# Performance work log

Hardware: AMD Instinct MI355X
Metric: run time of the kernel (lower is better)

## Reference

```python
import jax, jax.numpy as jnp
import numpy as np

HIDDEN = 2048
N_HEADS = 32
N_KV = 4
HEAD_DIM = 128
EPS = 1e-6
THETA = 1e6
B, S = 2, 2048


def setup_inputs() -> dict:
    key = jax.random.key(0)
    k1, k2, k3 = jax.random.split(key, 3)
    hidden_states = jax.random.normal(k1, (B, S, HIDDEN), dtype=jnp.float32)
    positions = jnp.broadcast_to(jnp.arange(S, dtype=jnp.int32), (B, S))
    w_qkv = jax.random.normal(k2, ((N_HEADS + 2 * N_KV) * HEAD_DIM, HIDDEN), dtype=jnp.float32) * 0.02
    w_o = jax.random.normal(k3, (HIDDEN, N_HEADS * HEAD_DIM), dtype=jnp.float32) * 0.02
    q_norm_w = jnp.ones((HEAD_DIM,), dtype=jnp.float32)
    k_norm_w = jnp.ones((HEAD_DIM,), dtype=jnp.float32)
    return {"hidden_states": hidden_states, "positions": positions,
            "w_qkv": w_qkv, "w_o": w_o, "q_norm_w": q_norm_w, "k_norm_w": k_norm_w}


def _rms_norm(x, w):
    # x: [..., HEAD_DIM]
    var = jnp.mean(x * x, axis=-1, keepdims=True)
    return x * jax.lax.rsqrt(var + EPS) * w


def _rope(x, positions):
    # NEOX-style rotary. x: [B,S,H,D], positions: [B,S]
    half = HEAD_DIM // 2
    inv_freq = 1.0 / (THETA ** (jnp.arange(0, half, dtype=jnp.float32) / half))
    ang = positions.astype(jnp.float32)[..., None] * inv_freq  # [B,S,half]
    cos = jnp.cos(ang)[:, :, None, :]
    sin = jnp.sin(ang)[:, :, None, :]
    x1, x2 = x[..., :half], x[..., half:]
    return jnp.concatenate([x1 * cos - x2 * sin, x2 * cos + x1 * sin], axis=-1)


def reference(hidden_states, positions, w_qkv, w_o, q_norm_w, k_norm_w):
    q_size = N_HEADS * HEAD_DIM
    kv_size = N_KV * HEAD_DIM
    qkv = jnp.einsum('bsh,oh->bso', hidden_states, w_qkv)
    q = qkv[..., :q_size].reshape(B, S, N_HEADS, HEAD_DIM)
    k = qkv[..., q_size:q_size + kv_size].reshape(B, S, N_KV, HEAD_DIM)
    v = qkv[..., q_size + kv_size:].reshape(B, S, N_KV, HEAD_DIM)
    # per-head RMSNorm then RoPE
    q = _rope(_rms_norm(q, q_norm_w), positions)
    k = _rope(_rms_norm(k, k_norm_w), positions)
    rep = N_HEADS // N_KV
    k = jnp.repeat(k, rep, axis=2)
    v = jnp.repeat(v, rep, axis=2)
    scale = HEAD_DIM ** -0.5
    scores = jnp.einsum('bqhd,bkhd->bhqk', q, k) * scale
    causal = jnp.tril(jnp.ones((S, S), dtype=bool))
    scores = jnp.where(causal, scores, jnp.finfo(scores.dtype).min)
    probs = jax.nn.softmax(scores, axis=-1)
    attn = jnp.einsum('bhqk,bkhd->bqhd', probs, v).reshape(B, S, N_HEADS * HEAD_DIM)
    return jnp.einsum('bsa,ha->bsh', attn, w_o)
```

## Files before the change

kernel.cpp:

```cpp
#include <hip/hip_runtime.h>
#include <cstdint>

#define SEQ 2048
#define BATCH 2
#define NTOK 4096
#define HID 2048
#define NH 32
#define NKV 4
#define HD 128
#define QKV_O 5120

typedef __attribute__((ext_vector_type(8))) short short8;
typedef __attribute__((ext_vector_type(8))) unsigned short u16x8;
typedef __attribute__((ext_vector_type(4))) unsigned short u16x4;
typedef __attribute__((ext_vector_type(4))) float f32x4;

__device__ __forceinline__ float bf2f(unsigned short u) {
  union { unsigned int i; float f; } v; v.i = ((unsigned int)u) << 16; return v.f;
}
__device__ __forceinline__ unsigned short f2bf(float f) {
  union { float f; unsigned int i; } v; v.f = f;
  unsigned int r = v.i + 0x7FFFu + ((v.i >> 16) & 1u);
  return (unsigned short)(r >> 16);
}

__device__ __forceinline__ void load_lds16(const void* g, void* l) {
  __builtin_amdgcn_global_load_lds((const __attribute__((address_space(1))) unsigned int*)g,
                                   (__attribute__((address_space(3))) unsigned int*)l, 16, 0, 0);
}

__global__ __launch_bounds__(256) void convert_to_bf16(const float* __restrict__ src,
                                                       unsigned short* __restrict__ dst,
                                                       int n4) {
  int i = blockIdx.x * blockDim.x + threadIdx.x;
  int stride = gridDim.x * blockDim.x;
  for (; i < n4; i += stride) {
    f32x4 v = *(const f32x4*)(src + 4 * (size_t)i);
    u16x4 o;
    o.x = f2bf(v.x); o.y = f2bf(v.y); o.z = f2bf(v.z); o.w = f2bf(v.w);
    *(u16x4*)(dst + 4 * (size_t)i) = o;
  }
}

__global__ __launch_bounds__(256) void reduce_add(float* __restrict__ out,
                                                  const float* __restrict__ part, int n4) {
  int i = blockIdx.x * blockDim.x + threadIdx.x;
  int stride = gridDim.x * blockDim.x;
  for (; i < n4; i += stride) {
    f32x4 a = *(const f32x4*)(out + 4 * (size_t)i);
    f32x4 b = *(const f32x4*)(part + 4 * (size_t)i);
    a.x += b.x; a.y += b.y; a.z += b.z; a.w += b.w;
    *(f32x4*)(out + 4 * (size_t)i) = a;
  }
}

template <bool OUT_F32, bool SPLIT>
__global__ __launch_bounds__(512, 2) void gemm256(
    const unsigned short* __restrict__ A, const unsigned short* __restrict__ B,
    void* __restrict__ C0, void* __restrict__ C1,
    int lda, int ldb, int ldc, int Kloop) {
  __shared__ alignas(16) unsigned short As[2][256 * 64];
  __shared__ alignas(16) unsigned short Bs[2][256 * 64];

  const int t = threadIdx.x;
  const int lane = t & 63, w = t >> 6;
  const int fr = lane & 15, g = lane >> 4;
  const int wm = w >> 2, wn = w & 3;
  const size_t m0 = (size_t)blockIdx.y * 256;
  const size_t n0 = (size_t)blockIdx.x * 256;
  const int kbase = SPLIT ? (int)blockIdx.z * Kloop : 0;
  void* Cv = (SPLIT && blockIdx.z) ? C1 : C0;

  const int srow = w * 8 + (lane >> 3);
  const int sch = (lane & 7) ^ ((lane >> 3) & 7);
  const unsigned short* gA[4];
  const unsigned short* gB[4];
#pragma unroll
  for (int i = 0; i < 4; i++) {
    gA[i] = A + (m0 + i * 64 + srow) * (size_t)lda + kbase + sch * 8;
    gB[i] = B + (n0 + i * 64 + srow) * (size_t)ldb + kbase + sch * 8;
  }

  auto stage = [&](int k0, int bi) {
#pragma unroll
    for (int i = 0; i < 4; i++) {
      load_lds16(gA[i] + k0, &As[bi][(i * 512 + w * 64) * 8]);
      load_lds16(gB[i] + k0, &Bs[bi][(i * 512 + w * 64) * 8]);
    }
  };

  f32x4 acc[8][4] = {};
  stage(0, 0);

  const int nk = Kloop / 64;
  for (int kt = 0; kt < nk; kt++) {
    const int cur = kt & 1;
    asm volatile("s_waitcnt vmcnt(0)" ::: "memory");
    __builtin_amdgcn_s_barrier();
    __builtin_amdgcn_sched_barrier(0);
    if (kt + 1 < nk) stage((kt + 1) * 64, cur ^ 1);

    const unsigned short* Ac = As[cur];
    const unsigned short* Bc = Bs[cur];

    short8 bfr[4][2];
#pragma unroll
    for (int nf = 0; nf < 4; nf++) {
      const int row = wn * 64 + nf * 16 + fr;
#pragma unroll
      for (int s = 0; s < 2; s++)
        bfr[nf][s] = *(const short8*)&Bc[row * 64 + (((s * 4 + g) ^ (fr & 7)) * 8)];
    }
    __builtin_amdgcn_s_setprio(1);
#pragma unroll
    for (int mf = 0; mf < 8; mf++) {
      const int row = wm * 128 + mf * 16 + fr;
      short8 af0 = *(const short8*)&Ac[row * 64 + (((0 + g) ^ (fr & 7)) * 8)];
      short8 af1 = *(const short8*)&Ac[row * 64 + (((4 + g) ^ (fr & 7)) * 8)];
#pragma unroll
      for (int nf = 0; nf < 4; nf++) {
        acc[mf][nf] = __builtin_amdgcn_mfma_f32_16x16x32_bf16(af0, bfr[nf][0], acc[mf][nf], 0, 0, 0);
        acc[mf][nf] = __builtin_amdgcn_mfma_f32_16x16x32_bf16(af1, bfr[nf][1], acc[mf][nf], 0, 0, 0);
      }
    }
    __builtin_amdgcn_s_setprio(0);
  }

#pragma unroll
  for (int mf = 0; mf < 8; mf++)
#pragma unroll
    for (int nf = 0; nf < 4; nf++) {
      size_t row = m0 + wm * 128 + mf * 16 + g * 4;
      size_t col = n0 + wn * 64 + nf * 16 + fr;
#pragma unroll
      for (int r = 0; r < 4; r++) {
        if (OUT_F32) ((float*)Cv)[(row + r) * ldc + col] = acc[mf][nf][r];
        else ((unsigned short*)Cv)[(row + r) * ldc + col] = f2bf(acc[mf][nf][r]);
      }
    }
}

template <bool OUT_F32>
__global__ __launch_bounds__(256) void gemm_bt_bf16(
    const unsigned short* __restrict__ A, const unsigned short* __restrict__ B,
    void* __restrict__ Cv, int lda, int ldb, int ldc, int K) {
  __shared__ alignas(16) unsigned short As[128 * 32];
  __shared__ alignas(16) unsigned short Bs[128 * 32];

  const int t    = threadIdx.x;
  const int lane = t & 63;
  const int w    = t >> 6;
  const int wm   = (w >> 1) * 64;
  const int wn   = (w & 1) * 64;
  const size_t m0 = (size_t)blockIdx.y * 128;
  const size_t n0 = (size_t)blockIdx.x * 128;

  f32x4 acc[4][4] = {};

  const int srow = w * 32 + (lane >> 2);
  const int scol = (lane & 3) * 8;
  const unsigned short* gA0 = &A[(m0 + srow) * (size_t)lda + scol];
  const unsigned short* gA1 = gA0 + 16 * (size_t)lda;
  const unsigned short* gB0 = &B[(n0 + srow) * (size_t)ldb + scol];
  const unsigned short* gB1 = gB0 + 16 * (size_t)ldb;
  unsigned short* lA0 = &As[(w * 32) * 32];
  unsigned short* lA1 = &As[(w * 32 + 16) * 32];
  unsigned short* lB0 = &Bs[(w * 32) * 32];
  unsigned short* lB1 = &Bs[(w * 32 + 16) * 32];

  const int fr = lane & 15;
  const int kb = (lane >> 4) * 8;

  for (int k0 = 0; k0 < K; k0 += 32) {
    load_lds16(gA0 + k0, lA0);
    load_lds16(gA1 + k0, lA1);
    load_lds16(gB0 + k0, lB0);
    load_lds16(gB1 + k0, lB1);
    __syncthreads();
    short8 af[4], bf[4];
#pragma unroll
    for (int mt = 0; mt < 4; mt++) af[mt] = *(const short8*)&As[(wm + mt * 16 + fr) * 32 + kb];
#pragma unroll
    for (int nt = 0; nt < 4; nt++) bf[nt] = *(const short8*)&Bs[(wn + nt * 16 + fr) * 32 + kb];
#pragma unroll
    for (int mt = 0; mt < 4; mt++)
#pragma unroll
      for (int nt = 0; nt < 4; nt++)
        acc[mt][nt] = __builtin_amdgcn_mfma_f32_16x16x32_bf16(af[mt], bf[nt], acc[mt][nt], 0, 0, 0);
    __syncthreads();
  }

  const int r4 = (lane >> 4) * 4;
  const int cc = lane & 15;
#pragma unroll
  for (int mt = 0; mt < 4; mt++)
#pragma unroll
    for (int nt = 0; nt < 4; nt++) {
      size_t row = m0 + wm + mt * 16 + r4;
      size_t col = n0 + wn + nt * 16 + cc;
#pragma unroll
      for (int r = 0; r < 4; r++) {
        if (OUT_F32) ((float*)Cv)[(row + r) * ldc + col] = acc[mt][nt][r];
        else ((unsigned short*)Cv)[(row + r) * ldc + col] = f2bf(acc[mt][nt][r]);
      }
    }
}

__global__ __launch_bounds__(64) void rope_tab(const int* __restrict__ pos,
                                               float2* __restrict__ tab) {
  const int tok = blockIdx.x;
  const int j = threadIdx.x;
  float p = (float)pos[tok];
  float inv_freq = expf((float)j * (-13.815510557964274f / 64.0f));
  float ang = p * inv_freq;
  float2 cs; cs.x = cosf(ang); cs.y = sinf(ang);
  tab[tok * 64 + j] = cs;
}

__global__ __launch_bounds__(256) void normrope(
    unsigned short* __restrict__ qkv, const float2* __restrict__ tab,
    const unsigned short* __restrict__ qw, const unsigned short* __restrict__ kw) {
  const int wv   = threadIdx.x >> 6;
  const int lane = threadIdx.x & 63;
  const int h    = blockIdx.x * 4 + wv;
  const int tok  = blockIdx.z * SEQ + blockIdx.y;

  const unsigned short* w = (h < NH) ? qw : kw;
  const size_t src = (size_t)tok * QKV_O + (size_t)h * HD;

  float x1 = bf2f(qkv[src + lane]);
  float x2 = bf2f(qkv[src + lane + 64]);
  float ss = x1 * x1 + x2 * x2;
#pragma unroll
  for (int off = 32; off; off >>= 1) ss += __shfl_xor(ss, off);
  float r = rsqrtf(ss * (1.0f / 128.0f) + 1e-6f);
  float n1 = x1 * r * bf2f(w[lane]);
  float n2 = x2 * r * bf2f(w[lane + 64]);

  float2 cs = tab[tok * 64 + lane];
  qkv[src + lane]      = f2bf(n1 * cs.x - n2 * cs.y);
  qkv[src + lane + 64] = f2bf(n2 * cs.x + n1 * cs.y);
}

__global__ __launch_bounds__(256) void transpose_v(const unsigned short* __restrict__ qkv,
                                                   unsigned short* __restrict__ vt) {
  __shared__ alignas(16) unsigned short Vs[64][136];
  const int k0 = blockIdx.x * 64, kvh = blockIdx.y, b = blockIdx.z;
  const int t = threadIdx.x;
  const int voff = (NH + NKV) * HD + kvh * HD;
  {
    const int row = t >> 2, cb = (t & 3) * 8;
    const size_t gb = (size_t)(b * SEQ + k0 + row) * QKV_O + voff;
#pragma unroll
    for (int r = 0; r < 4; r++)
      *(uint4*)&Vs[row][cb + 32 * r] = *(const uint4*)&qkv[gb + cb + 32 * r];
  }
  __syncthreads();
  const int d = t >> 1, half = t & 1;
  const size_t ob = ((size_t)((b * NKV + kvh) * HD + d)) * SEQ + k0 + half * 32;
#pragma unroll
  for (int i = 0; i < 4; i++) {
    u16x8 vv;
#pragma unroll
    for (int j = 0; j < 8; j++) vv[j] = Vs[half * 32 + i * 8 + j][d];
    *(u16x8*)&vt[ob + i * 8] = vv;
  }
}

__global__ __launch_bounds__(512, 4) void flash_mfma(unsigned short* __restrict__ qkv,
                                                     const unsigned short* __restrict__ vt) {
  __shared__ alignas(16) unsigned short Kbuf[2][64 * 128];
  __shared__ alignas(16) unsigned short Vbuf[2][128 * 64];
  __shared__ alignas(16) unsigned short Ps[8][16 * 64];

  const int p = (int)blockIdx.x;
  const int h = blockIdx.y, b = blockIdx.z;
  const int t = threadIdx.x;
  const int lane = t & 63, w = t >> 6;
  const int c = lane & 15, g = lane >> 4;
  const int kvh = h >> 3;
  const int koff = NH * HD + kvh * HD;
  const float scale = 0.08838834764831845f;
  const int swz = c & 7;
  const int nqt = SEQ / 128;

  const int rK0 = t >> 4,         jK0 = (t & 15) ^ (rK0 & 15);
  const int rK1 = (t + 512) >> 4, jK1 = ((t + 512) & 15) ^ (rK1 & 15);
  const int dV0 = t >> 3,         jV0 = (t & 7) ^ (dV0 & 7);
  const int dV1 = (t + 512) >> 3, jV1 = ((t + 512) & 7) ^ (dV1 & 7);
  const unsigned short* gK0 = qkv + (size_t)(b * SEQ + rK0) * QKV_O + koff + jK0 * 8;
  const unsigned short* gK1 = qkv + (size_t)(b * SEQ + rK1) * QKV_O + koff + jK1 * 8;
  const unsigned short* gV0 = vt + ((size_t)(b * NKV + kvh) * HD + dV0) * SEQ + jV0 * 8;
  const unsigned short* gV1 = vt + ((size_t)(b * NKV + kvh) * HD + dV1) * SEQ + jV1 * 8;

  auto stage = [&](int k0s, int bi) {
    load_lds16(gK0 + (size_t)k0s * QKV_O, &Kbuf[bi][(w * 64) * 8]);
    load_lds16(gK1 + (size_t)k0s * QKV_O, &Kbuf[bi][(w * 64 + 512) * 8]);
    load_lds16(gV0 + k0s, &Vbuf[bi][(w * 64) * 8]);
    load_lds16(gV1 + k0s, &Vbuf[bi][(w * 64 + 512) * 8]);
  };

  for (int job = 0; job < 2; job++) {
    const int qt = job == 0 ? (nqt - 1 - p) : p;
    const int q0 = qt * 128;
    const int nkt = 2 * qt + 2;

    stage(0, 0);

    short8 qf[4];
    {
      const size_t qr = (size_t)(b * SEQ + q0 + w * 16 + c) * QKV_O + (size_t)h * HD;
#pragma unroll
      for (int ks = 0; ks < 4; ks++)
        qf[ks] = *(const short8*)&qkv[qr + ks * 32 + g * 8];
    }

    f32x4 O[8] = {};
    float m_i = -1e30f, l_i = 0.0f;

    for (int kt = 0; kt < nkt; kt++) {
      const int cur = kt & 1;
      asm volatile("s_waitcnt vmcnt(0)" ::: "memory");
      __builtin_amdgcn_s_barrier();
      __builtin_amdgcn_sched_barrier(0);
      if (kt + 1 < nkt) stage((kt + 1) * 64, cur ^ 1);

      const unsigned short* Kc = Kbuf[cur];
      const unsigned short* Vc = Vbuf[cur];

      f32x4 sc[4];
#pragma unroll
      for (int mt = 0; mt < 4; mt++) sc[mt] = (f32x4){0.f, 0.f, 0.f, 0.f};
      __builtin_amdgcn_s_setprio(1);
#pragma unroll
      for (int ks = 0; ks < 4; ks++) {
#pragma unroll
        for (int mt = 0; mt < 4; mt++) {
          short8 kf = *(const short8*)&Kc[(mt * 16 + c) * 128 + (((ks * 4 + g) ^ c) * 8)];
          sc[mt] = __builtin_amdgcn_mfma_f32_16x16x32_bf16(kf, qf[ks], sc[mt], 0, 0, 0);
        }
      }
      __builtin_amdgcn_s_setprio(0);

      const int k0 = kt * 64;
      const int qrow = q0 + w * 16 + c;
      const bool need_mask = (k0 + 63 > q0 + w * 16);
      float mx = -3.0e38f;
#pragma unroll
      for (int mt = 0; mt < 4; mt++)
#pragma unroll
        for (int r = 0; r < 4; r++) {
          float s = sc[mt][r];
          if (need_mask && (k0 + mt * 16 + g * 4 + r > qrow)) s = -3.0e38f;
          sc[mt][r] = s;
          mx = fmaxf(mx, s);
        }
      mx = fmaxf(mx, __shfl_xor(mx, 16));
      mx = fmaxf(mx, __shfl_xor(mx, 32));
      float mxs = mx * scale;

      if (!__all(mxs - m_i <= 8.0f)) {
        float m_new = fmaxf(m_i, mxs);
        float alpha = __expf(m_i - m_new);
        f32x4 a4;
#pragma unroll
        for (int r = 0; r < 4; r++) a4[r] = __shfl(alpha, g * 4 + r);
#pragma unroll
        for (int nt = 0; nt < 8; nt++)
#pragma unroll
          for (int r = 0; r < 4; r++) O[nt][r] *= a4[r];
        l_i *= alpha;
        m_i = m_new;
      }

      float psum = 0.0f;
#pragma unroll
      for (int mt = 0; mt < 4; mt++) {
        float pv[4];
#pragma unroll
        for (int r = 0; r < 4; r++) {
          pv[r] = __expf(__builtin_fmaf(sc[mt][r], scale, -m_i));
          psum += pv[r];
        }
        unsigned int pk0, pk1;
        asm("v_cvt_pk_bf16_f32 %0, %1, %2" : "=v"(pk0) : "v"(pv[0]), "v"(pv[1]));
        asm("v_cvt_pk_bf16_f32 %0, %1, %2" : "=v"(pk1) : "v"(pv[2]), "v"(pv[3]));
        uint2 pk; pk.x = pk0; pk.y = pk1;
        *(uint2*)&Ps[w][c * 64 + (((mt * 2 + (g >> 1)) ^ swz) * 8) + (g & 1) * 4] = pk;
      }
      psum += __shfl_xor(psum, 16);
      psum += __shfl_xor(psum, 32);
      l_i += psum;

      __builtin_amdgcn_s_setprio(1);
#pragma unroll
      for (int ks = 0; ks < 2; ks++) {
        short8 pf = *(const short8*)&Ps[w][c * 64 + (((ks * 4 + g) ^ swz) * 8)];
#pragma unroll
        for (int nt = 0; nt < 8; nt++) {
          short8 vf = *(const short8*)&Vc[(nt * 16 + c) * 64 + (((ks * 4 + g) ^ swz) * 8)];
          O[nt] = __builtin_amdgcn_mfma_f32_16x16x32_bf16(pf, vf, O[nt], 0, 0, 0);
        }
      }
      __builtin_amdgcn_s_setprio(0);
    }

    f32x4 l4;
#pragma unroll
    for (int r = 0; r < 4; r++) l4[r] = __shfl(l_i, g * 4 + r);
    f32x4 li;
#pragma unroll
    for (int r = 0; r < 4; r++) li[r] = 1.0f / l4[r];
#pragma unroll
    for (int nt = 0; nt < 8; nt++)
#pragma unroll
      for (int r = 0; r < 4; r++) {
        size_t addr = (size_t)(b * SEQ + q0 + w * 16 + g * 4 + r) * QKV_O + h * HD + nt * 16 + c;
        qkv[addr] = f2bf(O[nt][r] * li[r]);
      }
  }
}

extern "C" void kernel_launch(void* const* d_in, const int* in_sizes, int n_in,
                              void* d_out, int out_size, void* d_ws, size_t ws_size,
                              hipStream_t stream) {
  const float* hidden_f = (const float*)d_in[0];
  const int* positions  = (const int*)d_in[1];
  const float* wqkv_f   = (const float*)d_in[2];
  const float* wo_f     = (const float*)d_in[3];
  const float* qn_f     = (const float*)d_in[4];
  const float* kn_f     = (const float*)d_in[5];
  float* out            = (float*)d_out;

  char* ws = (char*)d_ws;
  unsigned short* hidden_c = (unsigned short*)ws;
  unsigned short* wqkv_c   = (unsigned short*)(ws + 16777216);
  unsigned short* wo_c     = (unsigned short*)(ws + 37748736);
  unsigned short* qn_c     = (unsigned short*)(ws + 54525952);
  unsigned short* kn_c     = (unsigned short*)(ws + 54526208);
  unsigned short* qkv      = (unsigned short*)(ws + 54526464);
  unsigned short* vt_g     = (unsigned short*)(ws + 96469504);
  float2* rtab             = (float2*)ws;
  float* p0                = (float*)ws;

  convert_to_bf16<<<1024, 256, 0, stream>>>(hidden_f, hidden_c, NTOK * HID / 4);
  convert_to_bf16<<<1024, 256, 0, stream>>>(wqkv_f, wqkv_c, QKV_O * HID / 4);
  convert_to_bf16<<<1024, 256, 0, stream>>>(wo_f, wo_c, HID * NH * HD / 4);
  convert_to_bf16<<<1, 32, 0, stream>>>(qn_f, qn_c, HD / 4);
  convert_to_bf16<<<1, 32, 0, stream>>>(kn_f, kn_c, HD / 4);

  gemm256<false, false><<<dim3(NH * HD / 256, NTOK / 256), 512, 0, stream>>>(
      hidden_c, wqkv_c, qkv, qkv, HID, HID, QKV_O, HID);
  gemm_bt_bf16<false><<<dim3(2 * NKV * HD / 128, NTOK / 128), 256, 0, stream>>>(
      hidden_c, wqkv_c + (size_t)(NH * HD) * HID, qkv + NH * HD, HID, HID, QKV_O, HID);
  rope_tab<<<NTOK, 64, 0, stream>>>(positions, rtab);
  normrope<<<dim3((NH + NKV) / 4, SEQ, BATCH), 256, 0, stream>>>(qkv, rtab, qn_c, kn_c);
  transpose_v<<<dim3(SEQ / 64, NKV, BATCH), 256, 0, stream>>>(qkv, vt_g);
  flash_mfma<<<dim3(SEQ / 256, NH, BATCH), 512, 0, stream>>>(qkv, vt_g);
  gemm256<true, true><<<dim3(HID / 256, NTOK / 256, 2), 512, 0, stream>>>(
      qkv, wo_c, p0, out, QKV_O, NH * HD, HID, NH * HD / 2);
  reduce_add<<<2048, 256, 0, stream>>>(out, p0, NTOK * HID / 4);
}
```

Baseline: 468.0 us.

## Fuse bf16 conversions, skip fully-masked tiles, use exp2 softmax in flash attention

Merges the five fp32-to-bf16 conversion launches into one launch that picks its tensor by blockIdx.y, cutting launch overhead. In the flash attention loop, each wave now skips key tiles that lie entirely above its causal diagonal, and softmax uses exp2 with log2(e) folded into the scale. The row-max reduction is rewritten as a shallower tree and masking runs only when needed. Skipped waves still reach the loop's barriers because `continue` comes after the barrier and the stage call, so synchronization is preserved.

```diff
diff --git a/kernel.cpp b/kernel.cpp
--- a/kernel.cpp
+++ b/kernel.cpp
@@ -29,16 +29,27 @@
                                    (__attribute__((address_space(3))) unsigned int*)l, 16, 0, 0);
 }
 
-__global__ __launch_bounds__(256) void convert_to_bf16(const float* __restrict__ src,
-                                                       unsigned short* __restrict__ dst,
-                                                       int n4) {
+__global__ __launch_bounds__(256) void convert5(
+    const float* __restrict__ s0, unsigned short* __restrict__ d0, int n0,
+    const float* __restrict__ s1, unsigned short* __restrict__ d1, int n1,
+    const float* __restrict__ s2, unsigned short* __restrict__ d2, int n2,
+    const float* __restrict__ s3, unsigned short* __restrict__ d3, int n3,
+    const float* __restrict__ s4, unsigned short* __restrict__ d4, int n4_) {
+  const float* s; unsigned short* d; int n;
+  switch (blockIdx.y) {
+    case 0: s = s0; d = d0; n = n0; break;
+    case 1: s = s1; d = d1; n = n1; break;
+    case 2: s = s2; d = d2; n = n2; break;
+    case 3: s = s3; d = d3; n = n3; break;
+    default: s = s4; d = d4; n = n4_; break;
+  }
   int i = blockIdx.x * blockDim.x + threadIdx.x;
   int stride = gridDim.x * blockDim.x;
-  for (; i < n4; i += stride) {
-    f32x4 v = *(const f32x4*)(src + 4 * (size_t)i);
+  for (; i < n; i += stride) {
+    f32x4 v = *(const f32x4*)(s + 4 * (size_t)i);
     u16x4 o;
     o.x = f2bf(v.x); o.y = f2bf(v.y); o.z = f2bf(v.z); o.w = f2bf(v.w);
-    *(u16x4*)(dst + 4 * (size_t)i) = o;
+    *(u16x4*)(d + 4 * (size_t)i) = o;
   }
 }
 
@@ -280,7 +291,7 @@
   const int c = lane & 15, g = lane >> 4;
   const int kvh = h >> 3;
   const int koff = NH * HD + kvh * HD;
-  const float scale = 0.08838834764831845f;
+  const float scale2 = 0.12751744f;
   const int swz = c & 7;
   const int nqt = SEQ / 128;
 
@@ -325,6 +336,9 @@
       __builtin_amdgcn_sched_barrier(0);
       if (kt + 1 < nkt) stage((kt + 1) * 64, cur ^ 1);
 
+      const int k0 = kt * 64;
+      if (k0 > q0 + w * 16 + 15) continue;
+
       const unsigned short* Kc = Kbuf[cur];
       const unsigned short* Vc = Vbuf[cur];
 
@@ -342,26 +356,28 @@
       }
       __builtin_amdgcn_s_setprio(0);
 
-      const int k0 = kt * 64;
       const int qrow = q0 + w * 16 + c;
       const bool need_mask = (k0 + 63 > q0 + w * 16);
-      float mx = -3.0e38f;
-#pragma unroll
-      for (int mt = 0; mt < 4; mt++)
-#pragma unroll
-        for (int r = 0; r < 4; r++) {
-          float s = sc[mt][r];
-          if (need_mask && (k0 + mt * 16 + g * 4 + r > qrow)) s = -3.0e38f;
-          sc[mt][r] = s;
-          mx = fmaxf(mx, s);
-        }
+      if (need_mask) {
+#pragma unroll
+        for (int mt = 0; mt < 4; mt++)
+#pragma unroll
+          for (int r = 0; r < 4; r++)
+            if (k0 + mt * 16 + g * 4 + r > qrow) sc[mt][r] = -3.0e38f;
+      }
+      float ma = fmaxf(fmaxf(sc[0][0], sc[0][1]), sc[0][2]);
+      float mb = fmaxf(fmaxf(sc[0][3], sc[1][0]), sc[1][1]);
+      float mc = fmaxf(fmaxf(sc[1][2], sc[1][3]), sc[2][0]);
+      float md = fmaxf(fmaxf(sc[2][1], sc[2][2]), sc[2][3]);
+      float me = fmaxf(fmaxf(sc[3][0], sc[3][1]), sc[3][2]);
+      float mx = fmaxf(fmaxf(fmaxf(ma, mb), fmaxf(mc, md)), fmaxf(me, sc[3][3]));
       mx = fmaxf(mx, __shfl_xor(mx, 16));
       mx = fmaxf(mx, __shfl_xor(mx, 32));
-      float mxs = mx * scale;
-
-      if (!__all(mxs - m_i <= 8.0f)) {
-        float m_new = fmaxf(m_i, mxs);
-        float alpha = __expf(m_i - m_new);
+      float mx2 = mx * scale2;
+
+      if (!__all(mx2 - m_i <= 11.54156f)) {
+        float m_new = fmaxf(m_i, mx2);
+        float alpha = exp2f(m_i - m_new);
         f32x4 a4;
 #pragma unroll
         for (int r = 0; r < 4; r++) a4[r] = __shfl(alpha, g * 4 + r);
@@ -379,7 +395,7 @@
         float pv[4];
 #pragma unroll
         for (int r = 0; r < 4; r++) {
-          pv[r] = __expf(__builtin_fmaf(sc[mt][r], scale, -m_i));
+          pv[r] = exp2f(__builtin_fmaf(sc[mt][r], scale2, -m_i));
           psum += pv[r];
         }
         unsigned int pk0, pk1;
@@ -443,11 +459,12 @@
   float2* rtab             = (float2*)ws;
   float* p0                = (float*)ws;
 
-  convert_to_bf16<<<1024, 256, 0, stream>>>(hidden_f, hidden_c, NTOK * HID / 4);
-  convert_to_bf16<<<1024, 256, 0, stream>>>(wqkv_f, wqkv_c, QKV_O * HID / 4);
-  convert_to_bf16<<<1024, 256, 0, stream>>>(wo_f, wo_c, HID * NH * HD / 4);
-  convert_to_bf16<<<1, 32, 0, stream>>>(qn_f, qn_c, HD / 4);
-  convert_to_bf16<<<1, 32, 0, stream>>>(kn_f, kn_c, HD / 4);
+  convert5<<<dim3(512, 5), 256, 0, stream>>>(
+      hidden_f, hidden_c, NTOK * HID / 4,
+      wqkv_f, wqkv_c, QKV_O * HID / 4,
+      wo_f, wo_c, HID * NH * HD / 4,
+      qn_f, qn_c, HD / 4,
+      kn_f, kn_c, HD / 4);
 
   gemm256<false, false><<<dim3(NH * HD / 256, NTOK / 256), 512, 0, stream>>>(
       hidden_c, wqkv_c, qkv, qkv, HID, HID, QKV_O, HID);
```

After: 473.9 us. Within noise of the previous version (+1.2%).
